# Kernel tuning notes

Hardware: AMD Instinct MI355X
Metric: run time of the kernel (lower is better)

## Reference

```python
import jax, jax.numpy as jnp
import numpy as np

B, V, F, H, W = 2, 8000, 1500, 128, 128
EPS_AREA = 1e-8
EPS_Z = 1e-4


def setup_inputs() -> dict:
    key = jax.random.key(0)
    k1, k2, k3 = jax.random.split(key, 3)
    verts = jax.random.normal(k1, (B, V, 3), jnp.float32) * 0.5
    faces = jax.random.randint(k2, (F, 3), 0, V)
    R = jnp.tile(jnp.eye(3, dtype=jnp.float32)[None], (B, 1, 1)) + 0.01 * jax.random.normal(k3, (B, 3, 3), jnp.float32)
    T = jnp.tile(jnp.array([0.0, 0.0, 3.0], jnp.float32)[None], (B, 1))
    focal = jnp.float32(2.0)
    return {"verts": verts, "R": R, "T": T, "focal": focal, "faces": faces}


def _edge(ax, ay, bx, by, px, py):
    return (px - ax) * (by - ay) - (py - ay) * (bx - ax)


def _project(verts, R, T, focal):
    # world -> view -> screen (NDC xy); screen z replaced by view z (as in MeshRasterizer.transform)
    vv = jnp.einsum('bvi,bij->bvj', verts, R) + T[:, None, :]   # [B,V,3]
    z = vv[..., 2:3]
    xy = focal * vv[..., :2] / z
    return jnp.concatenate([xy, z], axis=-1)                     # [B,V,3]


def _rasterize(vs, faces):
    fv = vs[:, faces]                                            # [B,F,3,3] (vert, xyz)
    # PyTorch3D NDC pixel centers: +X left, +Y up
    xg = 1.0 - 2.0 * (jnp.arange(W, dtype=jnp.float32) + 0.5) / W
    yg = 1.0 - 2.0 * (jnp.arange(H, dtype=jnp.float32) + 0.5) / H
    pyy, pxx = jnp.meshgrid(yg, xg, indexing='ij')
    pxf, pyf = pxx.reshape(-1), pyy.reshape(-1)                  # [P]

    fx = fv[..., 0][:, None]                                     # [B,1,F,3]
    fy = fv[..., 1][:, None]
    fz = fv[..., 2][:, None]
    px = pxf[None, :, None]                                      # [1,P,1]
    py = pyf[None, :, None]

    area = _edge(fv[..., 0, 0], fv[..., 0, 1], fv[..., 1, 0], fv[..., 1, 1],
                 fv[..., 2, 0], fv[..., 2, 1])[:, None]          # [B,1,F]
    area_safe = jnp.where(jnp.abs(area) > EPS_AREA, area, EPS_AREA)

    w0 = _edge(fx[..., 1], fy[..., 1], fx[..., 2], fy[..., 2], px, py)
    w1 = _edge(fx[..., 2], fy[..., 2], fx[..., 0], fy[..., 0], px, py)
    w2 = _edge(fx[..., 0], fy[..., 0], fx[..., 1], fy[..., 1], px, py)
    b0, b1, b2 = w0 / area_safe, w1 / area_safe, w2 / area_safe  # [B,P,F]

    inside = (b0 >= 0) & (b1 >= 0) & (b2 >= 0) & (jnp.abs(area) > EPS_AREA)
    zp = b0 * fz[..., 0] + b1 * fz[..., 1] + b2 * fz[..., 2]     # [B,P,F]
    valid = inside & (zp > EPS_Z)

    zmask = jnp.where(valid, zp, jnp.inf)
    idx = jnp.argmin(zmask, axis=-1)                             # [B,P]
    zmin = jnp.min(zmask, axis=-1)
    hit = jnp.isfinite(zmin)                                     # [B,P]

    # gather winning face per pixel, recompute bary / z / dists only for it
    bfv = fv[jnp.arange(B)[:, None], idx]                        # [B,P,3,3]
    bx, by, bz = bfv[..., 0], bfv[..., 1], bfv[..., 2]           # [B,P,3]
    pxp, pyp = pxf[None, :], pyf[None, :]

    a2 = _edge(bx[..., 0], by[..., 0], bx[..., 1], by[..., 1], bx[..., 2], by[..., 2])
    a2s = jnp.where(jnp.abs(a2) > EPS_AREA, a2, EPS_AREA)
    c0 = _edge(bx[..., 1], by[..., 1], bx[..., 2], by[..., 2], pxp, pyp) / a2s
    c1 = _edge(bx[..., 2], by[..., 2], bx[..., 0], by[..., 0], pxp, pyp) / a2s
    c2 = _edge(bx[..., 0], by[..., 0], bx[..., 1], by[..., 1], pxp, pyp) / a2s
    bary = jnp.stack([c0, c1, c2], axis=-1)                      # [B,P,3]
    zbest = jnp.sum(bary * bz, axis=-1)                          # [B,P]

    def seg_d2(ax, ay, bx_, by_):
        dx, dy = bx_ - ax, by_ - ay
        l2 = jnp.maximum(dx * dx + dy * dy, 1e-12)
        t = jnp.clip(((pxp - ax) * dx + (pyp - ay) * dy) / l2, 0.0, 1.0)
        ex, ey = ax + t * dx - pxp, ay + t * dy - pyp
        return ex * ex + ey * ey

    d2 = jnp.minimum(jnp.minimum(
        seg_d2(bx[..., 0], by[..., 0], bx[..., 1], by[..., 1]),
        seg_d2(bx[..., 1], by[..., 1], bx[..., 2], by[..., 2])),
        seg_d2(bx[..., 2], by[..., 2], bx[..., 0], by[..., 0]))
    inside_b = (c0 >= 0) & (c1 >= 0) & (c2 >= 0)
    dists = jnp.where(inside_b, -d2, d2)                         # signed sq. distance

    neg1 = jnp.float32(-1.0)
    pix_to_face = jnp.where(hit, idx, -1).astype(jnp.int32).reshape(B, H, W, 1)
    zbuf = jnp.where(hit, zbest, neg1).reshape(B, H, W, 1)
    bary_o = jnp.where(hit[..., None], bary, neg1).reshape(B, H, W, 1, 3)
    dists_o = jnp.where(hit, dists, neg1).reshape(B, H, W, 1)
    return pix_to_face, zbuf, bary_o, dists_o


def reference(verts, R, T, focal, faces):
    vs = _project(verts, R, T, focal)
    return _rasterize(vs, faces)
```

## Files before the change

### kernel.cpp

```cpp
#include <hip/hip_runtime.h>
#include <math.h>

#pragma clang fp contract(off)

#define Bn 2
#define Vn 8000
#define Fn 1500
#define Hn 128
#define Wn 128
#define EPS_AREA_F 1e-8f
#define EPS_Z_F 1e-4f
#define NSEG 8
#define NSLICE 8
#define TPB (NSEG * 64)


__global__ void proj_kernel(const float* __restrict__ verts, const float* __restrict__ R,
                            const float* __restrict__ T, const float* __restrict__ focal,
                            const int* __restrict__ faces,
                            float4* __restrict__ recS, unsigned* __restrict__ bboxT) {
    int t = blockIdx.x * blockDim.x + threadIdx.x;
    if (t >= Bn * Fn) return;
    int b = t / Fn;
    int f = t - b * Fn;
    const float* Rb = R + b * 9;
    const float* Tb = T + b * 3;
    float fo = focal[0];
    float X[3], Y[3], Z[3];
    for (int k = 0; k < 3; ++k) {
        int vi = faces[f * 3 + k];
        const float* v = verts + ((size_t)b * Vn + vi) * 3;
        float v0 = v[0], v1 = v[1], v2 = v[2];
        float vx = v0 * Rb[0] + v1 * Rb[3] + v2 * Rb[6] + Tb[0];
        float vy = v0 * Rb[1] + v1 * Rb[4] + v2 * Rb[7] + Tb[1];
        float vz = v0 * Rb[2] + v1 * Rb[5] + v2 * Rb[8] + Tb[2];
        X[k] = (fo * vx) / vz;
        Y[k] = (fo * vy) / vz;
        Z[k] = vz;
    }
    float area = (X[2] - X[0]) * (Y[1] - Y[0]) - (Y[2] - Y[0]) * (X[1] - X[0]);
    float as = (fabsf(area) > EPS_AREA_F) ? area : EPS_AREA_F;
    recS[t * 3 + 0] = make_float4(X[0], Y[0], X[1], Y[1]);
    recS[t * 3 + 1] = make_float4(X[2], Y[2], area, as);
    recS[t * 3 + 2] = make_float4(Z[0], Z[1], Z[2], 0.0f);

    unsigned pk = 0xFFFFFFFFu;
    if (fabsf(area) > EPS_AREA_F) {
        float xmin = fminf(X[0], fminf(X[1], X[2]));
        float xmax = fmaxf(X[0], fmaxf(X[1], X[2]));
        float ymin = fminf(Y[0], fminf(Y[1], Y[2]));
        float ymax = fmaxf(Y[0], fmaxf(Y[1], Y[2]));
        const float D = 0.02f;
        float wlo = ceilf(64.0f * (1.0f - xmax - D) - 0.5f);
        float whi = floorf(64.0f * (1.0f - xmin + D) - 0.5f);
        float hlo = ceilf(64.0f * (1.0f - ymax - D) - 0.5f);
        float hhi = floorf(64.0f * (1.0f - ymin + D) - 0.5f);
        wlo = fmaxf(wlo, 0.0f); whi = fminf(whi, 127.0f);
        hlo = fmaxf(hlo, 0.0f); hhi = fminf(hhi, 127.0f);
        if ((wlo <= whi) && (hlo <= hhi)) {
            int tx0 = (int)wlo >> 3, tx1 = (int)whi >> 3;
            int ty0 = (int)hlo >> 3, ty1 = (int)hhi >> 3;
            pk = (unsigned)tx0 | ((unsigned)tx1 << 8) |
                 ((unsigned)ty0 << 16) | ((unsigned)ty1 << 24);
        }
    }
    bboxT[t] = pk;
}

__global__ __launch_bounds__(TPB)
void raster_kernel(const float4* __restrict__ recS, const unsigned* __restrict__ bboxT,
                   unsigned long long* __restrict__ keyslice) {
    __shared__ unsigned long long smK[NSEG * 64];

    int tid = threadIdx.x;
    int lane = tid & 63;
    int seg = tid >> 6;
    int blk = blockIdx.x;
    int slice = blk & (NSLICE - 1);
    int bt_ = blk >> 3;
    int b = bt_ >> 8;
    int tile = bt_ & 255;
    int ty = tile >> 4, tx = tile & 15;
    int h = (ty << 3) | (lane >> 3);
    int w = (tx << 3) | (lane & 7);
    float px = 1.0f - (2.0f * ((float)w + 0.5f)) / (float)Wn;
    float py = 1.0f - (2.0f * ((float)h + 0.5f)) / (float)Hn;

    int chunk = slice * NSEG + seg;
    int lo = (chunk * Fn) >> 6;
    int hi = ((chunk + 1) * Fn) >> 6;

    const unsigned* bbb = bboxT + (size_t)b * Fn;
    const float4* rb = recS + (size_t)b * Fn * 3;
    unsigned long long best = ~0ull;

    for (int f = lo; f < hi; ++f) {
        unsigned pk = bbb[f];
        if (pk == 0xFFFFFFFFu) continue;
        int tx0 = pk & 0xFF, tx1 = (pk >> 8) & 0xFF;
        int ty0 = (pk >> 16) & 0xFF, ty1 = (pk >> 24) & 0xFF;
        if (tx < tx0 || tx > tx1 || ty < ty0 || ty > ty1) continue;
        const float4* pr = rb + (size_t)f * 3;
        float4 q0 = pr[0];
        float4 q1 = pr[1];
        float x0 = q0.x, y0 = q0.y, x1 = q0.z, y1 = q0.w;
        float x2 = q1.x, y2 = q1.y, as = q1.w;
        float w0 = (px - x1) * (y2 - y1) - (py - y1) * (x2 - x1);
        float w1 = (px - x2) * (y0 - y2) - (py - y2) * (x0 - x2);
        float w2 = (px - x0) * (y1 - y0) - (py - y0) * (x1 - x0);
        bool ins = (as > 0.0f) ? (w0 >= 0.0f && w1 >= 0.0f && w2 >= 0.0f)
                               : (w0 <= 0.0f && w1 <= 0.0f && w2 <= 0.0f);
        if (ins) {
            float b0 = w0 / as;
            float b1 = w1 / as;
            float b2 = w2 / as;
            float4 q2 = pr[2];
            float zp = (b0 * q2.x + b1 * q2.y) + b2 * q2.z;
            if (zp > EPS_Z_F) {
                unsigned long long ck =
                    ((unsigned long long)__float_as_uint(zp) << 32) | (unsigned)f;
                if (ck < best) best = ck;
            }
        }
    }
    smK[seg * 64 + lane] = best;
    __syncthreads();

    if (tid < 64) {
        unsigned long long bk = smK[tid];
        #pragma unroll
        for (int s = 1; s < NSEG; ++s) {
            unsigned long long k = smK[s * 64 + tid];
            if (k < bk) bk = k;
        }
        int hh = (ty << 3) | (tid >> 3);
        int ww = (tx << 3) | (tid & 7);
        int p = (b << 14) + hh * Wn + ww;
        keyslice[(size_t)p * NSLICE + slice] = bk;
    }
}

__global__ __launch_bounds__(256)
void writer_kernel(const float4* __restrict__ recS,
                   const unsigned long long* __restrict__ keyslice,
                   float* __restrict__ out) {
    int p = blockIdx.x * blockDim.x + threadIdx.x;
    if (p >= Bn * Hn * Wn) return;
    int b = p >> 14;
    int hw = p & 16383;
    int h = hw >> 7;
    int w = hw & 127;
    float px = 1.0f - (2.0f * ((float)w + 0.5f)) / (float)Wn;
    float py = 1.0f - (2.0f * ((float)h + 0.5f)) / (float)Hn;
    const unsigned long long* ks = keyslice + (size_t)p * NSLICE;
    unsigned long long bk = ks[0];
    #pragma unroll
    for (int s = 1; s < NSLICE; ++s) {
        unsigned long long k = ks[s];
        if (k < bk) bk = k;
    }
    const float4* rb = recS + (size_t)b * Fn * 3;
    const int HWB = Bn * Hn * Wn;
    float o_idx = -1.0f, o_z = -1.0f, ob0 = -1.0f, ob1 = -1.0f, ob2 = -1.0f, o_d = -1.0f;
    if (bk != ~0ull) {
        int f = (int)(bk & 0xFFFFFFFFu);
        float4 q0 = rb[(size_t)f * 3 + 0];
        float4 q1 = rb[(size_t)f * 3 + 1];
        float x0 = q0.x, y0 = q0.y, x1 = q0.z, y1 = q0.w;
        float x2 = q1.x, y2 = q1.y, as = q1.w;
        float w0 = (px - x1) * (y2 - y1) - (py - y1) * (x2 - x1);
        float w1 = (px - x2) * (y0 - y2) - (py - y2) * (x0 - x2);
        float w2 = (px - x0) * (y1 - y0) - (py - y0) * (x1 - x0);
        float c0 = w0 / as, c1 = w1 / as, c2 = w2 / as;
        auto segd = [&](float ax, float ay, float bx, float by) -> float {
            float dx = bx - ax, dy = by - ay;
            float l2 = dx * dx + dy * dy;
            l2 = (l2 > 1e-12f) ? l2 : 1e-12f;
            float q = ((px - ax) * dx + (py - ay) * dy) / l2;
            q = (q < 0.0f) ? 0.0f : ((q > 1.0f) ? 1.0f : q);
            float ex = (ax + q * dx) - px;
            float ey = (ay + q * dy) - py;
            return ex * ex + ey * ey;
        };
        float d2 = fminf(fminf(segd(x0, y0, x1, y1), segd(x1, y1, x2, y2)),
                         segd(x2, y2, x0, y0));
        bool inside_b = (c0 >= 0.0f) && (c1 >= 0.0f) && (c2 >= 0.0f);
        o_idx = (float)f;
        o_z = __uint_as_float((unsigned)(bk >> 32));
        ob0 = c0; ob1 = c1; ob2 = c2;
        o_d = inside_b ? -d2 : d2;
    }
    out[p] = o_idx;
    out[HWB + p] = o_z;
    out[2 * HWB + p * 3 + 0] = ob0;
    out[2 * HWB + p * 3 + 1] = ob1;
    out[2 * HWB + p * 3 + 2] = ob2;
    out[5 * HWB + p] = o_d;
}

extern "C" void kernel_launch(void* const* d_in, const int* in_sizes, int n_in,
                              void* d_out, int out_size, void* d_ws, size_t ws_size,
                              hipStream_t stream) {
    const float* verts = (const float*)d_in[0];
    const float* R     = (const float*)d_in[1];
    const float* T     = (const float*)d_in[2];
    const float* focal = (const float*)d_in[3];
    const int*   faces = (const int*)d_in[4];
    float* out = (float*)d_out;
    char* ws = (char*)d_ws;
    float4* recS                 = (float4*)(ws);
    unsigned* bboxT              = (unsigned*)(ws + 144000);
    unsigned long long* keyslice = (unsigned long long*)(ws + 156000);

    hipLaunchKernelGGL(proj_kernel, dim3((Bn * Fn + 255) / 256), dim3(256), 0, stream,
                       verts, R, T, focal, faces, recS, bboxT);
    hipLaunchKernelGGL(raster_kernel, dim3(Bn * 256 * NSLICE), dim3(TPB), 0, stream,
                       recS, bboxT, keyslice);
    hipLaunchKernelGGL(writer_kernel, dim3((Bn * Hn * Wn + 255) / 256), dim3(256),
                       0, stream, recS, keyslice, out);
}
```

Before: 98.41 us.

## Cull faces per tile cooperatively and stage surviving records in LDS

Each raster block now tests all faces of its slice against the tile bbox at once, using ballot and an atomic counter to compact the survivors into a shared list. The survivors' records are then staged in LDS, and the eight wave segments stride over that compact list. Before, each wave walked its own face range serially and loaded records from global memory. This aims to remove serial bbox checks and repeated global loads, and to balance work across waves. The cost is extra barriers and an LDS copy, and MAXR=192 assumes a slice holds at most 188 faces, which holds for these sizes.

New measurement: 85.38 us (median of 2 runs). -13.2%, faster.

```diff
diff --git a/kernel.cpp b/kernel.cpp
--- a/kernel.cpp
+++ b/kernel.cpp
@@ -13,6 +13,7 @@
 #define NSEG 8
 #define NSLICE 8
 #define TPB (NSEG * 64)
+#define MAXR 192
 
 
 __global__ void proj_kernel(const float* __restrict__ verts, const float* __restrict__ R,
@@ -70,7 +71,10 @@
 __global__ __launch_bounds__(TPB)
 void raster_kernel(const float4* __restrict__ recS, const unsigned* __restrict__ bboxT,
                    unsigned long long* __restrict__ keyslice) {
+    __shared__ unsigned short smList[MAXR];
+    __shared__ float4 smRec[MAXR * 3];
     __shared__ unsigned long long smK[NSEG * 64];
+    __shared__ int smCount;
 
     int tid = threadIdx.x;
     int lane = tid & 63;
@@ -81,28 +85,56 @@
     int b = bt_ >> 8;
     int tile = bt_ & 255;
     int ty = tile >> 4, tx = tile & 15;
+
+    int lo = (slice * Fn) >> 3;
+    int hi = ((slice + 1) * Fn) >> 3;
+    int n = hi - lo;
+
+    if (tid == 0) smCount = 0;
+    __syncthreads();
+
+    {
+        bool pass = false;
+        if (tid < n) {
+            unsigned pk = bboxT[(size_t)b * Fn + lo + tid];
+            if (pk != 0xFFFFFFFFu) {
+                int tx0 = pk & 0xFF, tx1 = (pk >> 8) & 0xFF;
+                int ty0 = (pk >> 16) & 0xFF, ty1 = (pk >> 24) & 0xFF;
+                pass = (tx >= tx0) & (tx <= tx1) & (ty >= ty0) & (ty <= ty1);
+            }
+        }
+        unsigned long long m = __ballot(pass);
+        int cnt = (int)__popcll(m);
+        if (cnt) {
+            int base = 0;
+            if (lane == 0) base = atomicAdd(&smCount, cnt);
+            base = __shfl(base, 0);
+            if (pass) {
+                int pos = (int)__popcll(m & ((1ull << lane) - 1ull));
+                smList[base + pos] = (unsigned short)(lo + tid);
+            }
+        }
+    }
+    __syncthreads();
+    int cnt = smCount;
+
+    for (int i = tid; i < cnt * 3; i += TPB) {
+        int f = smList[i / 3];
+        smRec[i] = recS[((size_t)b * Fn + f) * 3 + (i - (i / 3) * 3)];
+    }
+    __syncthreads();
+
     int h = (ty << 3) | (lane >> 3);
     int w = (tx << 3) | (lane & 7);
     float px = 1.0f - (2.0f * ((float)w + 0.5f)) / (float)Wn;
     float py = 1.0f - (2.0f * ((float)h + 0.5f)) / (float)Hn;
 
-    int chunk = slice * NSEG + seg;
-    int lo = (chunk * Fn) >> 6;
-    int hi = ((chunk + 1) * Fn) >> 6;
-
-    const unsigned* bbb = bboxT + (size_t)b * Fn;
-    const float4* rb = recS + (size_t)b * Fn * 3;
     unsigned long long best = ~0ull;
-
-    for (int f = lo; f < hi; ++f) {
-        unsigned pk = bbb[f];
-        if (pk == 0xFFFFFFFFu) continue;
-        int tx0 = pk & 0xFF, tx1 = (pk >> 8) & 0xFF;
-        int ty0 = (pk >> 16) & 0xFF, ty1 = (pk >> 24) & 0xFF;
-        if (tx < tx0 || tx > tx1 || ty < ty0 || ty > ty1) continue;
-        const float4* pr = rb + (size_t)f * 3;
-        float4 q0 = pr[0];
-        float4 q1 = pr[1];
+    for (int j = seg; j < cnt; j += NSEG) {
+        float4 q0 = smRec[j * 3 + 0];
+        float4 q1 = smRec[j * 3 + 1];
+        float4 q2 = smRec[j * 3 + 2];
+        int f = smList[j];
         float x0 = q0.x, y0 = q0.y, x1 = q0.z, y1 = q0.w;
         float x2 = q1.x, y2 = q1.y, as = q1.w;
         float w0 = (px - x1) * (y2 - y1) - (py - y1) * (x2 - x1);
@@ -114,7 +146,6 @@
             float b0 = w0 / as;
             float b1 = w1 / as;
             float b2 = w2 / as;
-            float4 q2 = pr[2];
             float zp = (b0 * q2.x + b1 * q2.y) + b2 * q2.z;
             if (zp > EPS_Z_F) {
                 unsigned long long ck =
```
